# Kernel tuning notes

Hardware: AMD Instinct MI355X
Metric: run time of the kernel (lower is better)

Reference implementation:

```python
import jax, jax.numpy as jnp
import numpy as np

# E2M1 (FP4) representable magnitudes and rounding midpoints
LEVELS = jnp.array([0.0, 0.5, 1.0, 1.5, 2.0, 3.0, 4.0, 6.0], dtype=jnp.float32)
BOUNDS = jnp.array([0.25, 0.75, 1.25, 1.75, 2.5, 3.5, 5.0], dtype=jnp.float32)
E2M1_MAX = 6.0
EPS = 1e-12


def e2m1_block_quant_dequant(x, block_size):
    """Block-wise E2M1 fake-quantization along the last dim.

    Per block of `block_size` elements: scale = absmax / 6.0, then
    round-to-nearest onto the E2M1 grid {0,.5,1,1.5,2,3,4,6} (signed)
    and dequantize. Returns (dequantized x, per-block scales).
    """
    shape = x.shape
    nb = shape[-1] // block_size
    xb = x.reshape(*shape[:-1], nb, block_size)
    amax = jnp.max(jnp.abs(xb), axis=-1, keepdims=True)          # [..., nb, 1]
    scale = jnp.maximum(amax / E2M1_MAX, EPS)
    v = xb / scale
    mag = jnp.abs(v)
    # nearest E2M1 level: count how many rounding boundaries |v| exceeds
    idx = jnp.sum((mag[..., None] > BOUNDS).astype(jnp.int32), axis=-1)
    q = jnp.sign(v) * LEVELS[idx] * scale                        # dequantized
    return q.reshape(shape), scale[..., 0]


def setup_inputs() -> dict:
    key = jax.random.key(0)
    k1, k2, k3 = jax.random.split(key, 3)
    x = jax.random.normal(k1, (8, 1500, 1280), dtype=jnp.float32)
    weight = jax.random.normal(k2, (5120, 1280), dtype=jnp.float32) * 0.02
    bias = jax.random.normal(k3, (5120,), dtype=jnp.float32) * 0.01
    return {"x": x, "weight": weight, "bias": bias}


def reference(x, weight, bias):
    # activation quant (block_size_act = 32, along feature dim)
    x_q, _ = e2m1_block_quant_dequant(x, 32)
    # weight quant (block_size_w = 32, along in_features dim)
    w_q, scale_w = e2m1_block_quant_dequant(weight, 32)
    # F.linear: x @ W^T + b
    out = jnp.einsum('bsi,oi->bso', x_q, w_q) + bias
    return (out, scale_w)
```

## Files before the change

kernel.cpp:

```cpp
#include <hip/hip_runtime.h>
#include <hip/hip_fp16.h>


typedef _Float16 f16;
typedef _Float16 f16x8 __attribute__((ext_vector_type(8)));
typedef float f32x4 __attribute__((ext_vector_type(4)));

#define M_ROWS 12000
#define M_PAD  12032
#define N_COLS 5120
#define K_DIM  1280
#define KB     40
#define NT     40
#define NTN    20

#define BAR()   asm volatile("s_barrier" ::: "memory")
#define LGKM0() asm volatile("s_waitcnt lgkmcnt(0)" ::: "memory")
#define VMCNT(N) asm volatile("s_waitcnt vmcnt(%0)" :: "i"(N) : "memory")
#define GLDS(gp, lp) __builtin_amdgcn_global_load_lds( \
    (const __attribute__((address_space(1))) unsigned*)(gp), \
    (__attribute__((address_space(3))) unsigned*)(lp), 16, 0, 0)

__device__ __forceinline__ float e2m1_level(float a) {
    float lv;
    if (a > 2.5f)       lv = (a > 3.5f) ? ((a > 5.0f) ? 6.0f : 4.0f) : 3.0f;
    else if (a > 1.25f) lv = (a > 1.75f) ? 2.0f : 1.5f;
    else                lv = (a > 0.75f) ? 1.0f : ((a > 0.25f) ? 0.5f : 0.0f);
    return lv;
}

__global__ __launch_bounds__(256) void quant_x_kernel(const float* __restrict__ x,
                                                      f16* __restrict__ xq) {
    int t = blockIdx.x * blockDim.x + threadIdx.x;
    int row = t / 160;
    int c8  = t % 160;
    f16x8 o;
    if (row < M_ROWS) {
        const float* p = x + (size_t)row * K_DIM + c8 * 8;
        float v[8];
        *(float4*)&v[0] = *(const float4*)p;
        *(float4*)&v[4] = *(const float4*)(p + 4);
        float am = 0.0f;
        #pragma unroll
        for (int i = 0; i < 8; ++i) am = fmaxf(am, fabsf(v[i]));
        am = fmaxf(am, __shfl_xor(am, 1));
        am = fmaxf(am, __shfl_xor(am, 2));
        float scale = fmaxf(am / 6.0f, 1e-12f);
        #pragma unroll
        for (int i = 0; i < 8; ++i) {
            float tq = v[i] / scale;
            float q  = copysignf(e2m1_level(fabsf(tq)), tq) * scale;
            o[i] = (f16)q;
        }
    } else {
        #pragma unroll
        for (int i = 0; i < 8; ++i) o[i] = (f16)0.0f;
    }
    *(f16x8*)(xq + (size_t)row * K_DIM + c8 * 8) = o;
}

__global__ __launch_bounds__(256) void quant_w_kernel(const float* __restrict__ w,
                                                      f16* __restrict__ wq,
                                                      float* __restrict__ scale_out) {
    int t = blockIdx.x * blockDim.x + threadIdx.x;
    int row = t / 160;
    int c8  = t % 160;
    const float* p = w + (size_t)row * K_DIM + c8 * 8;
    float v[8];
    *(float4*)&v[0] = *(const float4*)p;
    *(float4*)&v[4] = *(const float4*)(p + 4);
    float am = 0.0f;
    #pragma unroll
    for (int i = 0; i < 8; ++i) am = fmaxf(am, fabsf(v[i]));
    am = fmaxf(am, __shfl_xor(am, 1));
    am = fmaxf(am, __shfl_xor(am, 2));
    float scale = fmaxf(am / 6.0f, 1e-12f);
    if ((t & 3) == 0) scale_out[row * KB + (c8 >> 2)] = scale;
    f16x8 o;
    #pragma unroll
    for (int i = 0; i < 8; ++i) {
        float tq = v[i] / scale;
        float q  = copysignf(e2m1_level(fabsf(tq)), tq) * scale;
        o[i] = (f16)q;
    }
    *(f16x8*)(wq + (size_t)row * K_DIM + c8 * 8) = o;
}


__device__ __forceinline__ void stage_A32(const f16* __restrict__ g, f16* l, int tid) {
    int r = tid >> 2;
    int c = (tid & 3) ^ ((r >> 1) & 3);
    GLDS(g + (size_t)r * K_DIM + c * 8, l + (size_t)tid * 8);
}
__device__ __forceinline__ void stage_B32(const f16* __restrict__ g, f16* l, int tid, int h) {
    int rr  = tid >> 2;
    int row = (rr & 31) + ((rr >> 5) << 6) + (h << 5);
    int c   = (tid & 3) ^ ((row >> 1) & 3);
    GLDS(g + (size_t)row * K_DIM + c * 8, l + (size_t)(row * 4 + (tid & 3)) * 8);
}

template<int VM, bool S1, bool S2>
__device__ __forceinline__ void ktile(const f16* Ab, const f16* Bb, f16* oBb,
                                      f16* Ab_w, f16* Bb_w,
                                      const f16* gA2, const f16* gB2, const f16* gB1,
                                      f32x4 (&acc)[4][4],
                                      int tid, int arow0, int brow0, int swzc) {
    f16x8 a[4], bl[2], bh[2];

    LGKM0();
    VMCNT(VM);
    BAR();
    if (S1) stage_B32(gB1, oBb, tid, 1);
    #pragma unroll
    for (int fm = 0; fm < 4; ++fm)
        a[fm] = *(const f16x8*)&Ab[(arow0 + fm * 16) * 32 + swzc];
    #pragma unroll
    for (int fn = 0; fn < 2; ++fn)
        bl[fn] = *(const f16x8*)&Bb[(brow0 + fn * 16) * 32 + swzc];
    __builtin_amdgcn_s_setprio(1);
    #pragma unroll
    for (int fm = 0; fm < 4; ++fm)
        #pragma unroll
        for (int fn = 0; fn < 2; ++fn)
            acc[fm][fn] = __builtin_amdgcn_mfma_f32_16x16x32_f16(a[fm], bl[fn], acc[fm][fn], 0, 0, 0);
    __builtin_amdgcn_s_setprio(0);

    LGKM0();
    BAR();
    if (S2) { stage_A32(gA2, Ab_w, tid); stage_B32(gB2, Bb_w, tid, 0); }
    #pragma unroll
    for (int fn = 0; fn < 2; ++fn)
        bh[fn] = *(const f16x8*)&Bb[(brow0 + 32 + fn * 16) * 32 + swzc];
    __builtin_amdgcn_s_setprio(1);
    #pragma unroll
    for (int fm = 0; fm < 4; ++fm)
        #pragma unroll
        for (int fn = 0; fn < 2; ++fn)
            acc[fm][fn + 2] = __builtin_amdgcn_mfma_f32_16x16x32_f16(a[fm], bh[fn], acc[fm][fn + 2], 0, 0, 0);
    __builtin_amdgcn_s_setprio(0);
}

__global__ __launch_bounds__(512, 4) void gemm_kernel(const f16* __restrict__ A,
                                                      const f16* __restrict__ B,
                                                      const float* __restrict__ bias,
                                                      float* __restrict__ C) {
    __shared__ f16 sm[24576];
    f16* A0 = sm;
    f16* B0 = sm + 4096;
    f16* A1 = sm + 12288;
    f16* B1 = sm + 16384;

    int mt = blockIdx.x / NTN;
    int nt = blockIdx.x % NTN;

    int tid  = threadIdx.x;
    int lane = tid & 63;
    int wid  = tid >> 6;
    int wr   = wid >> 2;
    int wc   = wid & 3;
    int l15  = lane & 15;

    int swzc  = (((lane >> 4) ^ ((l15 >> 1) & 3)) << 3);
    int arow0 = wr * 64 + l15;
    int brow0 = wc * 64 + l15;

    const f16* gAb = A + (size_t)(mt * 128) * K_DIM;
    const f16* gBb = B + (size_t)(nt * 256) * K_DIM;

    f32x4 acc[4][4] = {};

    stage_A32(gAb,      A0, tid);
    stage_B32(gBb,      B0, tid, 0);
    stage_B32(gBb,      B0, tid, 1);
    stage_A32(gAb + 32, A1, tid);
    stage_B32(gBb + 32, B1, tid, 0);

    for (int tt = 0; tt < 19; ++tt) {
        int t = 2 * tt;
        ktile<2, true, true>(A0, B0, B1, A0, B0,
                             gAb + (t + 2) * 32, gBb + (t + 2) * 32, gBb + (t + 1) * 32,
                             acc, tid, arow0, brow0, swzc);
        ktile<2, true, true>(A1, B1, B0, A1, B1,
                             gAb + (t + 3) * 32, gBb + (t + 3) * 32, gBb + (t + 2) * 32,
                             acc, tid, arow0, brow0, swzc);
    }
    ktile<2, true, false>(A0, B0, B1, A0, B0, gAb, gBb, gBb + 39 * 32,
                          acc, tid, arow0, brow0, swzc);
    ktile<0, false, false>(A1, B1, B0, A1, B1, gAb, gBb, gBb,
                           acc, tid, arow0, brow0, swzc);

    int crow0 = mt * 128 + wr * 64;
    int ccol  = nt * 256 + wc * 64 + l15;
    float bz[4];
    #pragma unroll
    for (int fn = 0; fn < 4; ++fn) bz[fn] = bias[ccol + fn * 16];

    #pragma unroll
    for (int fm = 0; fm < 4; ++fm) {
        #pragma unroll
        for (int j = 0; j < 4; ++j) {
            int row = crow0 + fm * 16 + (lane >> 4) * 4 + j;
            if (row < M_ROWS) {
                float* cp = C + (size_t)row * N_COLS + ccol;
                #pragma unroll
                for (int fn = 0; fn < 4; ++fn)
                    cp[fn * 16] = acc[fm][fn][j] + bz[fn];
            }
        }
    }
}

extern "C" void kernel_launch(void* const* d_in, const int* in_sizes, int n_in,
                              void* d_out, int out_size, void* d_ws, size_t ws_size,
                              hipStream_t stream) {
    const float* x      = (const float*)d_in[0];
    const float* weight = (const float*)d_in[1];
    const float* bias   = (const float*)d_in[2];
    float* out     = (float*)d_out;
    float* scale_w = (float*)d_out + (size_t)M_ROWS * N_COLS;

    f16* xq = (f16*)d_ws;
    f16* wq = (f16*)((char*)d_ws + (size_t)M_PAD * K_DIM * sizeof(f16));

    {
        int threads = M_PAD * (K_DIM / 8);
        quant_x_kernel<<<threads / 256, 256, 0, stream>>>(x, xq);
    }
    {
        int threads = N_COLS * (K_DIM / 8);
        quant_w_kernel<<<threads / 256, 256, 0, stream>>>(weight, wq, scale_w);
    }
    {
        int grid = (M_PAD / 128) * (N_COLS / 256);
        gemm_kernel<<<grid, 512, 0, stream>>>(xq, wq, bias, out);
    }
}
```

Before: 216.0 us.

## Prefetch next k-tile fragments into registers and use one barrier per tile

```diff
diff --git a/kernel.cpp b/kernel.cpp
--- a/kernel.cpp
+++ b/kernel.cpp
@@ -11,11 +11,10 @@
 #define N_COLS 5120
 #define K_DIM  1280
 #define KB     40
-#define NT     40
 #define NTN    20
 
 #define BAR()   asm volatile("s_barrier" ::: "memory")
-#define LGKM0() asm volatile("s_waitcnt lgkmcnt(0)" ::: "memory")
+#define LGKM(N) asm volatile("s_waitcnt lgkmcnt(%0)" :: "i"(N) : "memory")
 #define VMCNT(N) asm volatile("s_waitcnt vmcnt(%0)" :: "i"(N) : "memory")
 #define GLDS(gp, lp) __builtin_amdgcn_global_load_lds( \
     (const __attribute__((address_space(1))) unsigned*)(gp), \
@@ -92,51 +91,55 @@
     int c = (tid & 3) ^ ((r >> 1) & 3);
     GLDS(g + (size_t)r * K_DIM + c * 8, l + (size_t)tid * 8);
 }
-__device__ __forceinline__ void stage_B32(const f16* __restrict__ g, f16* l, int tid, int h) {
-    int rr  = tid >> 2;
-    int row = (rr & 31) + ((rr >> 5) << 6) + (h << 5);
-    int c   = (tid & 3) ^ ((row >> 1) & 3);
-    GLDS(g + (size_t)row * K_DIM + c * 8, l + (size_t)(row * 4 + (tid & 3)) * 8);
-}
-
-template<int VM, bool S1, bool S2>
-__device__ __forceinline__ void ktile(const f16* Ab, const f16* Bb, f16* oBb,
-                                      f16* Ab_w, f16* Bb_w,
-                                      const f16* gA2, const f16* gB2, const f16* gB1,
+__device__ __forceinline__ void stage_B32f(const f16* __restrict__ g, f16* l, int tid) {
+    #pragma unroll
+    for (int s = 0; s < 2; ++s) {
+        int j   = s * 512 + tid;
+        int row = j >> 2;
+        int c   = (j & 3) ^ ((row >> 1) & 3);
+        GLDS(g + (size_t)row * K_DIM + c * 8, l + (size_t)j * 8);
+    }
+}
+
+template<int PAR, bool STAGE, bool READNEXT>
+__device__ __forceinline__ void ktile(const f16* Xa, const f16* Xb,
+                                      f16* Wa, f16* Wb,
+                                      const f16* Ya, const f16* Yb,
+                                      const f16* gA2, const f16* gB2,
+                                      f16x8 (&aF)[2][4], f16x8 (&blF)[2][2],
                                       f32x4 (&acc)[4][4],
                                       int tid, int arow0, int brow0, int swzc) {
-    f16x8 a[4], bl[2], bh[2];
-
-    LGKM0();
-    VMCNT(VM);
+    f16x8 bh[2];
+    #pragma unroll
+    for (int fn = 0; fn < 2; ++fn)
+        bh[fn] = *(const f16x8*)&Xb[(brow0 + 32 + fn * 16) * 32 + swzc];
+    LGKM(2);
+    __builtin_amdgcn_s_setprio(1);
+    #pragma unroll
+    for (int fm = 0; fm < 4; ++fm)
+        #pragma unroll
+        for (int fn = 0; fn < 2; ++fn)
+            acc[fm][fn] = __builtin_amdgcn_mfma_f32_16x16x32_f16(aF[PAR][fm], blF[PAR][fn], acc[fm][fn], 0, 0, 0);
+    __builtin_amdgcn_s_setprio(0);
+
+    VMCNT(0);
+    LGKM(0);
     BAR();
-    if (S1) stage_B32(gB1, oBb, tid, 1);
+    if (STAGE) { stage_A32(gA2, Wa, tid); stage_B32f(gB2, Wb, tid); }
+    if (READNEXT) {
+        #pragma unroll
+        for (int fm = 0; fm < 4; ++fm)
+            aF[1 - PAR][fm] = *(const f16x8*)&Ya[(arow0 + fm * 16) * 32 + swzc];
+        #pragma unroll
+        for (int fn = 0; fn < 2; ++fn)
+            blF[1 - PAR][fn] = *(const f16x8*)&Yb[(brow0 + fn * 16) * 32 + swzc];
+    }
+    __builtin_amdgcn_s_setprio(1);
     #pragma unroll
     for (int fm = 0; fm < 4; ++fm)
-        a[fm] = *(const f16x8*)&Ab[(arow0 + fm * 16) * 32 + swzc];
-    #pragma unroll
-    for (int fn = 0; fn < 2; ++fn)
-        bl[fn] = *(const f16x8*)&Bb[(brow0 + fn * 16) * 32 + swzc];
-    __builtin_amdgcn_s_setprio(1);
-    #pragma unroll
-    for (int fm = 0; fm < 4; ++fm)
         #pragma unroll
         for (int fn = 0; fn < 2; ++fn)
-            acc[fm][fn] = __builtin_amdgcn_mfma_f32_16x16x32_f16(a[fm], bl[fn], acc[fm][fn], 0, 0, 0);
-    __builtin_amdgcn_s_setprio(0);
-
-    LGKM0();
-    BAR();
-    if (S2) { stage_A32(gA2, Ab_w, tid); stage_B32(gB2, Bb_w, tid, 0); }
-    #pragma unroll
-    for (int fn = 0; fn < 2; ++fn)
-        bh[fn] = *(const f16x8*)&Bb[(brow0 + 32 + fn * 16) * 32 + swzc];
-    __builtin_amdgcn_s_setprio(1);
-    #pragma unroll
-    for (int fm = 0; fm < 4; ++fm)
-        #pragma unroll
-        for (int fn = 0; fn < 2; ++fn)
-            acc[fm][fn + 2] = __builtin_amdgcn_mfma_f32_16x16x32_f16(a[fm], bh[fn], acc[fm][fn + 2], 0, 0, 0);
+            acc[fm][fn + 2] = __builtin_amdgcn_mfma_f32_16x16x32_f16(aF[PAR][fm], bh[fn], acc[fm][fn + 2], 0, 0, 0);
     __builtin_amdgcn_s_setprio(0);
 }
 
@@ -168,26 +171,34 @@
     const f16* gBb = B + (size_t)(nt * 256) * K_DIM;
 
     f32x4 acc[4][4] = {};
-
-    stage_A32(gAb,      A0, tid);
-    stage_B32(gBb,      B0, tid, 0);
-    stage_B32(gBb,      B0, tid, 1);
-    stage_A32(gAb + 32, A1, tid);
-    stage_B32(gBb + 32, B1, tid, 0);
+    f16x8 aF[2][4], blF[2][2];
+
+    stage_A32(gAb,       A0, tid);
+    stage_B32f(gBb,      B0, tid);
+    stage_A32(gAb + 32,  A1, tid);
+    stage_B32f(gBb + 32, B1, tid);
+    VMCNT(3);
+    BAR();
+    #pragma unroll
+    for (int fm = 0; fm < 4; ++fm)
+        aF[0][fm] = *(const f16x8*)&A0[(arow0 + fm * 16) * 32 + swzc];
+    #pragma unroll
+    for (int fn = 0; fn < 2; ++fn)
+        blF[0][fn] = *(const f16x8*)&B0[(brow0 + fn * 16) * 32 + swzc];
 
     for (int tt = 0; tt < 19; ++tt) {
         int t = 2 * tt;
-        ktile<2, true, true>(A0, B0, B1, A0, B0,
-                             gAb + (t + 2) * 32, gBb + (t + 2) * 32, gBb + (t + 1) * 32,
-                             acc, tid, arow0, brow0, swzc);
-        ktile<2, true, true>(A1, B1, B0, A1, B1,
-                             gAb + (t + 3) * 32, gBb + (t + 3) * 32, gBb + (t + 2) * 32,
-                             acc, tid, arow0, brow0, swzc);
-    }
-    ktile<2, true, false>(A0, B0, B1, A0, B0, gAb, gBb, gBb + 39 * 32,
-                          acc, tid, arow0, brow0, swzc);
-    ktile<0, false, false>(A1, B1, B0, A1, B1, gAb, gBb, gBb,
-                           acc, tid, arow0, brow0, swzc);
+        ktile<0, true, true>(A0, B0, A0, B0, A1, B1,
+                             gAb + (t + 2) * 32, gBb + (t + 2) * 32,
+                             aF, blF, acc, tid, arow0, brow0, swzc);
+        ktile<1, true, true>(A1, B1, A1, B1, A0, B0,
+                             gAb + (t + 3) * 32, gBb + (t + 3) * 32,
+                             aF, blF, acc, tid, arow0, brow0, swzc);
+    }
+    ktile<0, false, true>(A0, B0, A0, B0, A1, B1, gAb, gBb,
+                          aF, blF, acc, tid, arow0, brow0, swzc);
+    ktile<1, false, false>(A1, B1, A1, B1, A0, B0, gAb, gBb,
+                           aF, blF, acc, tid, arow0, brow0, swzc);
 
     int crow0 = mt * 128 + wr * 64;
     int ccol  = nt * 256 + wc * 64 + l15;
```

Result: slower. 231.9 us (+7.4%).
